# Performance work log

Hardware: AMD Instinct MI355X
Metric: run time of the kernel (lower is better)

## Reference

```python
import jax, jax.numpy as jnp
import numpy as np

B, K, NS, NT = 4, 16, 4096, 16384
TEMPERATURE = 1.0


def setup_inputs() -> dict:
    key = jax.random.key(0)
    k1, k2, k3 = jax.random.split(key, 3)
    return {
        "sem_logits": jax.random.normal(k1, (B, K, NS), dtype=jnp.float32),
        "source_pos": jax.random.normal(k2, (B, 3, NS), dtype=jnp.float32),
        "target_pos": jax.random.normal(k3, (B, 3, NT), dtype=jnp.float32),
    }


def reference(sem_logits, source_pos, target_pos):
    # temperature scaling
    x = sem_logits / max(1e-06, TEMPERATURE)
    # use_max_class=True: per-point max over class logits -> [B, 1, Ns]
    src_feat = jnp.max(x, axis=1, keepdims=True)

    # nearest neighbor via squared euclidean distance (argmin matches cdist+top-1)
    t = jnp.swapaxes(target_pos, 1, 2)  # [B, Nt, 3]
    s = jnp.swapaxes(source_pos, 1, 2)  # [B, Ns, 3]
    d2 = (
        jnp.sum(t * t, axis=-1, keepdims=True)        # [B, Nt, 1]
        + jnp.sum(s * s, axis=-1)[:, None, :]          # [B, 1, Ns]
        - 2.0 * jnp.einsum("bnd,bmd->bnm", t, s)      # [B, Nt, Ns]
    )
    nn_idx = jnp.argmin(d2, axis=-1)  # [B, Nt]

    # gather: torch's source_feat[batch_idx, :, nn_idx] yields [B, Nt, C]
    gathered = jnp.take_along_axis(src_feat, nn_idx[:, None, :], axis=2)  # [B, 1, Nt]
    out = jnp.swapaxes(gathered, 1, 2)  # [B, Nt, 1]
    return jax.nn.sigmoid(out)
```

## Files before the change

### kernel.cpp

```cpp
#include <hip/hip_runtime.h>
#include <math.h>
#include <float.h>

#define BATCH 4
#define KCLS 16
#define NSRC 4096
#define NTGT 16384

#define THREADS 512
#define WAVES 8
#define TPL 8
#define TGT_PER_BLOCK 512
#define SPLITS 8
#define CHUNK (NSRC / SPLITS)
#define STRIPE (CHUNK / WAVES)

__global__ __launch_bounds__(THREADS) void nn_partial_kernel(
    const float* __restrict__ source_pos,
    const float* __restrict__ target_pos,
    unsigned long long* __restrict__ ws64)
{
    __shared__ float4 ls[TGT_PER_BLOCK * WAVES / 2];

    int tid = threadIdx.x;
    int lane = tid & 63;
    int wave = tid >> 6;

    int b = blockIdx.x >> 8;
    int rem = blockIdx.x & 255;
    int tg = rem >> 3;
    int split = rem & 7;
    int tbase = tg * TGT_PER_BLOCK;
    int cg = split * CHUNK;

    const float* sxp = source_pos + (size_t)b * 3 * NSRC;
    const float* syp = sxp + NSRC;
    const float* szp = sxp + 2 * NSRC;
    {
        int s = tid;
        float x = sxp[cg + s], y = syp[cg + s], z = szp[cg + s];
        float ss = __fadd_rn(__fadd_rn(__fmul_rn(x, x), __fmul_rn(y, y)),
                             __fmul_rn(z, z));
        ls[s] = make_float4(x, y, z, ss);
    }

    const float* tp = target_pos + (size_t)b * 3 * NTGT;
    float tx[TPL], ty[TPL], tz[TPL], tt[TPL];
#pragma unroll
    for (int j = 0; j < TPL; ++j) {
        int t = tbase + 64 * j + lane;
        tx[j] = tp[t]; ty[j] = tp[NTGT + t]; tz[j] = tp[2 * NTGT + t];
        tt[j] = __fadd_rn(__fadd_rn(__fmul_rn(tx[j], tx[j]),
                                    __fmul_rn(ty[j], ty[j])),
                          __fmul_rn(tz[j], tz[j]));
    }

    __syncthreads();

    int lbase = wave * STRIPE;
    int gbase = cg + lbase;
    float best[TPL];
    int bi[TPL];
#pragma unroll
    for (int j = 0; j < TPL; ++j) { best[j] = FLT_MAX; bi[j] = 0; }

#pragma unroll 8
    for (int i = 0; i < STRIPE; ++i) {
        float4 f = ls[lbase + i];
        int cand = gbase + i;
#pragma unroll
        for (int j = 0; j < TPL; ++j) {
            float acc = __fmul_rn(tx[j], f.x);
            acc = __fmaf_rn(ty[j], f.y, acc);
            acc = __fmaf_rn(tz[j], f.z, acc);
            float d2 = __fmaf_rn(-2.0f, acc, __fadd_rn(tt[j], f.w));
            if (d2 < best[j]) { best[j] = d2; bi[j] = cand; }
        }
    }

    __syncthreads();

    float* smin = (float*)ls;
    int* sidx = (int*)(smin + WAVES * TGT_PER_BLOCK);
#pragma unroll
    for (int j = 0; j < TPL; ++j) {
        smin[wave * TGT_PER_BLOCK + 64 * j + lane] = best[j];
        sidx[wave * TGT_PER_BLOCK + 64 * j + lane] = bi[j];
    }
    __syncthreads();

    {
        int t = tid;
        float m = smin[t];
        int mi = sidx[t];
#pragma unroll
        for (int j = 1; j < WAVES; ++j) {
            float mj = smin[j * TGT_PER_BLOCK + t];
            int ij = sidx[j * TGT_PER_BLOCK + t];
            if (mj < m || (mj == m && ij < mi)) { m = mj; mi = ij; }
        }
        unsigned u = __float_as_uint(m);
        unsigned ord = (u & 0x80000000u) ? ~u : (u | 0x80000000u);
        unsigned long long packed =
            ((unsigned long long)ord << 32) | (unsigned)mi;
        atomicMin(&ws64[(size_t)b * NTGT + tbase + t], packed);
    }
}

__global__ __launch_bounds__(256) void gate_kernel(
    const unsigned long long* __restrict__ ws64,
    const float* __restrict__ sem_logits,
    float* __restrict__ out)
{
    int gt = blockIdx.x * 256 + threadIdx.x;
    int b = gt / NTGT;
    int mi = (int)(ws64[gt] & 0xFFFFFFFFull);

    const float* lg = sem_logits + (size_t)b * KCLS * NSRC + mi;
    float mm = lg[0];
#pragma unroll
    for (int k = 1; k < KCLS; ++k) mm = fmaxf(mm, lg[(size_t)k * NSRC]);
    out[gt] = 1.0f / (1.0f + expf(-mm));
}

extern "C" void kernel_launch(void* const* d_in, const int* in_sizes, int n_in,
                              void* d_out, int out_size, void* d_ws, size_t ws_size,
                              hipStream_t stream) {
    const float* sem_logits = (const float*)d_in[0];
    const float* source_pos = (const float*)d_in[1];
    const float* target_pos = (const float*)d_in[2];
    float* out = (float*)d_out;

    unsigned long long* ws64 = (unsigned long long*)d_ws;

    hipMemsetAsync(ws64, 0xFF, sizeof(unsigned long long) * BATCH * NTGT, stream);

    nn_partial_kernel<<<BATCH * (NTGT / TGT_PER_BLOCK) * SPLITS, THREADS, 0, stream>>>(
        source_pos, target_pos, ws64);
    gate_kernel<<<(BATCH * NTGT) / 256, 256, 0, stream>>>(ws64, sem_logits, out);
}
```

Measured before the change: 100.0 us.

## Prepack sources and max-logits, stream sources via scalar loads, drop atomics

Adds a pack kernel that builds x,y,z plus squared norm for each source once, and also precomputes the per-source max over the class logits. The NN kernel then reads source points straight from global memory through a wave-uniform pointer (readfirstlane), so they can go through scalar loads, with a simple register double-buffer in place of the shared-memory staging and its barrier. Each split writes its partial argmin to its own slot, which replaces the memset and the 64-bit atomicMin; the gate kernel reduces the 8 partials and reads the precomputed max-logit. The cost is an extra launch, larger workspace traffic, and a prefetch that reads slightly past the end of each stripe.

```diff
diff --git a/kernel.cpp b/kernel.cpp
--- a/kernel.cpp
+++ b/kernel.cpp
@@ -15,12 +15,40 @@
 #define CHUNK (NSRC / SPLITS)
 #define STRIPE (CHUNK / WAVES)
 
-__global__ __launch_bounds__(THREADS) void nn_partial_kernel(
+#define WS_PACKED 0
+#define WS_MAXLOG (BATCH * NSRC * 16)
+#define WS_PART   (WS_MAXLOG + BATCH * NSRC * 4)
+
+__global__ __launch_bounds__(256) void pack_kernel(
     const float* __restrict__ source_pos,
+    const float* __restrict__ sem_logits,
+    float4* __restrict__ packed,
+    float* __restrict__ maxlog)
+{
+    int g = blockIdx.x * 256 + threadIdx.x;
+    int b = g >> 12;
+    int s = g & (NSRC - 1);
+
+    const float* sxp = source_pos + (size_t)b * 3 * NSRC;
+    float x = sxp[s], y = sxp[NSRC + s], z = sxp[2 * NSRC + s];
+    float ss = __fadd_rn(__fadd_rn(__fmul_rn(x, x), __fmul_rn(y, y)),
+                         __fmul_rn(z, z));
+    packed[g] = make_float4(x, y, z, ss);
+
+    const float* lg = sem_logits + (size_t)b * KCLS * NSRC + s;
+    float mm = lg[0];
+#pragma unroll
+    for (int k = 1; k < KCLS; ++k) mm = fmaxf(mm, lg[(size_t)k * NSRC]);
+    maxlog[g] = mm;
+}
+
+__global__ __launch_bounds__(THREADS) void nn_kernel(
+    const float4* __restrict__ packed,
     const float* __restrict__ target_pos,
-    unsigned long long* __restrict__ ws64)
+    unsigned long long* __restrict__ part)
 {
-    __shared__ float4 ls[TGT_PER_BLOCK * WAVES / 2];
+    __shared__ float smin[WAVES * TGT_PER_BLOCK];
+    __shared__ int   sidx[WAVES * TGT_PER_BLOCK];
 
     int tid = threadIdx.x;
     int lane = tid & 63;
@@ -33,17 +61,6 @@
     int tbase = tg * TGT_PER_BLOCK;
     int cg = split * CHUNK;
 
-    const float* sxp = source_pos + (size_t)b * 3 * NSRC;
-    const float* syp = sxp + NSRC;
-    const float* szp = sxp + 2 * NSRC;
-    {
-        int s = tid;
-        float x = sxp[cg + s], y = syp[cg + s], z = szp[cg + s];
-        float ss = __fadd_rn(__fadd_rn(__fmul_rn(x, x), __fmul_rn(y, y)),
-                             __fmul_rn(z, z));
-        ls[s] = make_float4(x, y, z, ss);
-    }
-
     const float* tp = target_pos + (size_t)b * 3 * NTGT;
     float tx[TPL], ty[TPL], tz[TPL], tt[TPL];
 #pragma unroll
@@ -55,33 +72,39 @@
                           __fmul_rn(tz[j], tz[j]));
     }
 
-    __syncthreads();
+    int gbase = cg + wave * STRIPE;
+    int ubase = __builtin_amdgcn_readfirstlane(gbase);
+    const float4* sp = packed + (size_t)b * NSRC + ubase;
 
-    int lbase = wave * STRIPE;
-    int gbase = cg + lbase;
     float best[TPL];
     int bi[TPL];
 #pragma unroll
     for (int j = 0; j < TPL; ++j) { best[j] = FLT_MAX; bi[j] = 0; }
 
-#pragma unroll 8
-    for (int i = 0; i < STRIPE; ++i) {
-        float4 f = ls[lbase + i];
-        int cand = gbase + i;
+    float4 cur[4], nxt[4];
 #pragma unroll
-        for (int j = 0; j < TPL; ++j) {
-            float acc = __fmul_rn(tx[j], f.x);
-            acc = __fmaf_rn(ty[j], f.y, acc);
-            acc = __fmaf_rn(tz[j], f.z, acc);
-            float d2 = __fmaf_rn(-2.0f, acc, __fadd_rn(tt[j], f.w));
-            if (d2 < best[j]) { best[j] = d2; bi[j] = cand; }
+    for (int k = 0; k < 4; ++k) cur[k] = sp[k];
+
+    for (int i0 = 0; i0 < STRIPE; i0 += 4) {
+#pragma unroll
+        for (int k = 0; k < 4; ++k) nxt[k] = sp[i0 + 4 + k];
+#pragma unroll
+        for (int k = 0; k < 4; ++k) {
+            float4 f = cur[k];
+            int cand = gbase + i0 + k;
+#pragma unroll
+            for (int j = 0; j < TPL; ++j) {
+                float acc = __fmul_rn(tx[j], f.x);
+                acc = __fmaf_rn(ty[j], f.y, acc);
+                acc = __fmaf_rn(tz[j], f.z, acc);
+                float d2 = __fmaf_rn(-2.0f, acc, __fadd_rn(tt[j], f.w));
+                if (d2 < best[j]) { best[j] = d2; bi[j] = cand; }
+            }
         }
+#pragma unroll
+        for (int k = 0; k < 4; ++k) cur[k] = nxt[k];
     }
 
-    __syncthreads();
-
-    float* smin = (float*)ls;
-    int* sidx = (int*)(smin + WAVES * TGT_PER_BLOCK);
 #pragma unroll
     for (int j = 0; j < TPL; ++j) {
         smin[wave * TGT_PER_BLOCK + 64 * j + lane] = best[j];
@@ -94,32 +117,37 @@
         float m = smin[t];
         int mi = sidx[t];
 #pragma unroll
-        for (int j = 1; j < WAVES; ++j) {
-            float mj = smin[j * TGT_PER_BLOCK + t];
-            int ij = sidx[j * TGT_PER_BLOCK + t];
+        for (int w = 1; w < WAVES; ++w) {
+            float mj = smin[w * TGT_PER_BLOCK + t];
+            int ij = sidx[w * TGT_PER_BLOCK + t];
             if (mj < m || (mj == m && ij < mi)) { m = mj; mi = ij; }
         }
         unsigned u = __float_as_uint(m);
         unsigned ord = (u & 0x80000000u) ? ~u : (u | 0x80000000u);
-        unsigned long long packed =
+        part[((size_t)b * SPLITS + split) * NTGT + tbase + t] =
             ((unsigned long long)ord << 32) | (unsigned)mi;
-        atomicMin(&ws64[(size_t)b * NTGT + tbase + t], packed);
     }
 }
 
 __global__ __launch_bounds__(256) void gate_kernel(
-    const unsigned long long* __restrict__ ws64,
-    const float* __restrict__ sem_logits,
+    const unsigned long long* __restrict__ part,
+    const float* __restrict__ maxlog,
     float* __restrict__ out)
 {
     int gt = blockIdx.x * 256 + threadIdx.x;
-    int b = gt / NTGT;
-    int mi = (int)(ws64[gt] & 0xFFFFFFFFull);
+    int b = gt >> 14;
+    int t = gt & (NTGT - 1);
 
-    const float* lg = sem_logits + (size_t)b * KCLS * NSRC + mi;
-    float mm = lg[0];
+    const unsigned long long* pp = part + (size_t)b * SPLITS * NTGT + t;
+    unsigned long long best = pp[0];
 #pragma unroll
-    for (int k = 1; k < KCLS; ++k) mm = fmaxf(mm, lg[(size_t)k * NSRC]);
+    for (int s = 1; s < SPLITS; ++s) {
+        unsigned long long v = pp[(size_t)s * NTGT];
+        if (v < best) best = v;
+    }
+    int mi = (int)(best & 0xFFFFFFFFull);
+
+    float mm = maxlog[(b << 12) + mi];
     out[gt] = 1.0f / (1.0f + expf(-mm));
 }
 
@@ -131,11 +159,14 @@
     const float* target_pos = (const float*)d_in[2];
     float* out = (float*)d_out;
 
-    unsigned long long* ws64 = (unsigned long long*)d_ws;
+    char* ws = (char*)d_ws;
+    float4* packed = (float4*)(ws + WS_PACKED);
+    float* maxlog = (float*)(ws + WS_MAXLOG);
+    unsigned long long* part = (unsigned long long*)(ws + WS_PART);
 
-    hipMemsetAsync(ws64, 0xFF, sizeof(unsigned long long) * BATCH * NTGT, stream);
-
-    nn_partial_kernel<<<BATCH * (NTGT / TGT_PER_BLOCK) * SPLITS, THREADS, 0, stream>>>(
-        source_pos, target_pos, ws64);
-    gate_kernel<<<(BATCH * NTGT) / 256, 256, 0, stream>>>(ws64, sem_logits, out);
+    pack_kernel<<<(BATCH * NSRC) / 256, 256, 0, stream>>>(
+        source_pos, sem_logits, packed, maxlog);
+    nn_kernel<<<BATCH * (NTGT / TGT_PER_BLOCK) * SPLITS, THREADS, 0, stream>>>(
+        packed, target_pos, part);
+    gate_kernel<<<(BATCH * NTGT) / 256, 256, 0, stream>>>(part, maxlog, out);
 }
```

After: 114.6 us. 1.15x slower.

## Replace atomicMin merge with per-split partial buffers and halve source splits

Applied to the files above, without the earlier changes.

Each nearest-neighbour block now writes its packed (distance, index) result to its own per-split slot, and the gate kernel reduces the splits itself. This removes the memset launch and the 64-bit global atomics. The source split count also drops from 8 to 4, so each block loads a larger source chunk into shared memory and the grid has half as many blocks. In exchange, occupancy may fall because shared memory per block grows and fewer blocks cover the GPU's CUs.

```diff
diff --git a/kernel.cpp b/kernel.cpp
--- a/kernel.cpp
+++ b/kernel.cpp
@@ -11,33 +11,35 @@
 #define WAVES 8
 #define TPL 8
 #define TGT_PER_BLOCK 512
-#define SPLITS 8
+#define SPLITS 4
 #define CHUNK (NSRC / SPLITS)
 #define STRIPE (CHUNK / WAVES)
 
-__global__ __launch_bounds__(THREADS) void nn_partial_kernel(
+
+__global__ __launch_bounds__(THREADS) void nn_kernel(
     const float* __restrict__ source_pos,
     const float* __restrict__ target_pos,
-    unsigned long long* __restrict__ ws64)
+    unsigned long long* __restrict__ part)
 {
-    __shared__ float4 ls[TGT_PER_BLOCK * WAVES / 2];
+    __shared__ float4 ls[CHUNK * 2];
 
     int tid = threadIdx.x;
     int lane = tid & 63;
     int wave = tid >> 6;
 
-    int b = blockIdx.x >> 8;
-    int rem = blockIdx.x & 255;
-    int tg = rem >> 3;
-    int split = rem & 7;
+    int b = blockIdx.x >> 7;
+    int rem = blockIdx.x & 127;
+    int tg = rem >> 2;
+    int split = rem & 3;
     int tbase = tg * TGT_PER_BLOCK;
     int cg = split * CHUNK;
 
     const float* sxp = source_pos + (size_t)b * 3 * NSRC;
     const float* syp = sxp + NSRC;
     const float* szp = sxp + 2 * NSRC;
-    {
-        int s = tid;
+#pragma unroll
+    for (int r = 0; r < CHUNK / THREADS; ++r) {
+        int s = r * THREADS + tid;
         float x = sxp[cg + s], y = syp[cg + s], z = szp[cg + s];
         float ss = __fadd_rn(__fadd_rn(__fmul_rn(x, x), __fmul_rn(y, y)),
                              __fmul_rn(z, z));
@@ -94,27 +96,35 @@
         float m = smin[t];
         int mi = sidx[t];
 #pragma unroll
-        for (int j = 1; j < WAVES; ++j) {
-            float mj = smin[j * TGT_PER_BLOCK + t];
-            int ij = sidx[j * TGT_PER_BLOCK + t];
+        for (int w = 1; w < WAVES; ++w) {
+            float mj = smin[w * TGT_PER_BLOCK + t];
+            int ij = sidx[w * TGT_PER_BLOCK + t];
             if (mj < m || (mj == m && ij < mi)) { m = mj; mi = ij; }
         }
         unsigned u = __float_as_uint(m);
         unsigned ord = (u & 0x80000000u) ? ~u : (u | 0x80000000u);
-        unsigned long long packed =
+        part[((size_t)b * SPLITS + split) * NTGT + tbase + t] =
             ((unsigned long long)ord << 32) | (unsigned)mi;
-        atomicMin(&ws64[(size_t)b * NTGT + tbase + t], packed);
     }
 }
 
 __global__ __launch_bounds__(256) void gate_kernel(
-    const unsigned long long* __restrict__ ws64,
+    const unsigned long long* __restrict__ part,
     const float* __restrict__ sem_logits,
     float* __restrict__ out)
 {
     int gt = blockIdx.x * 256 + threadIdx.x;
-    int b = gt / NTGT;
-    int mi = (int)(ws64[gt] & 0xFFFFFFFFull);
+    int b = gt >> 14;
+    int t = gt & (NTGT - 1);
+
+    const unsigned long long* pp = part + (size_t)b * SPLITS * NTGT + t;
+    unsigned long long best = pp[0];
+#pragma unroll
+    for (int s = 1; s < SPLITS; ++s) {
+        unsigned long long v = pp[(size_t)s * NTGT];
+        if (v < best) best = v;
+    }
+    int mi = (int)(best & 0xFFFFFFFFull);
 
     const float* lg = sem_logits + (size_t)b * KCLS * NSRC + mi;
     float mm = lg[0];
@@ -131,11 +141,9 @@
     const float* target_pos = (const float*)d_in[2];
     float* out = (float*)d_out;
 
-    unsigned long long* ws64 = (unsigned long long*)d_ws;
+    unsigned long long* part = (unsigned long long*)d_ws;
 
-    hipMemsetAsync(ws64, 0xFF, sizeof(unsigned long long) * BATCH * NTGT, stream);
-
-    nn_partial_kernel<<<BATCH * (NTGT / TGT_PER_BLOCK) * SPLITS, THREADS, 0, stream>>>(
-        source_pos, target_pos, ws64);
-    gate_kernel<<<(BATCH * NTGT) / 256, 256, 0, stream>>>(ws64, sem_logits, out);
+    nn_kernel<<<BATCH * (NTGT / TGT_PER_BLOCK) * SPLITS, THREADS, 0, stream>>>(
+        source_pos, target_pos, part);
+    gate_kernel<<<(BATCH * NTGT) / 256, 256, 0, stream>>>(part, sem_logits, out);
 }
```

New measurement: 100.5 us. About the same (+0.5%).
